# Kernel tuning notes

Measured on AMD Instinct MI355X. Metric: run time of the kernel, lower is better.

The kernel has to match this reference:

```python
import jax, jax.numpy as jnp
import numpy as np

DIM = 1024
NUM_HEADS = 16
HEAD_DIM = DIM // NUM_HEADS
ROPE_BASE = 10000.0


def _rope_cos_sin(seq_len, head_dim, dtype):
    inv_freq = 1.0 / (ROPE_BASE ** (jnp.arange(0, head_dim, 2, dtype=jnp.float32) / head_dim))
    t = jnp.arange(seq_len, dtype=jnp.float32)
    freqs = jnp.einsum('i,j->ij', t, inv_freq)          # (S, head_dim/2)
    emb = jnp.concatenate([freqs, freqs], axis=-1)       # (S, head_dim)
    return jnp.cos(emb).astype(dtype), jnp.sin(emb).astype(dtype)


def _rotate_half(x):
    x1, x2 = jnp.split(x, 2, axis=-1)
    return jnp.concatenate([-x2, x1], axis=-1)


def setup_inputs() -> dict:
    key = jax.random.key(0)
    k1, k2, k3 = jax.random.split(key, 3)
    B, S = 2, 2048
    x = jax.random.normal(k1, (B, S, DIM), dtype=jnp.float32)
    w_qkv = jax.random.normal(k2, (3 * DIM, DIM), dtype=jnp.float32) * (DIM ** -0.5)
    w_out = jax.random.normal(k3, (DIM, DIM), dtype=jnp.float32) * (DIM ** -0.5)
    return {"x": x, "w_qkv": w_qkv, "w_out": w_out}


def reference(x, w_qkv, w_out):
    B, S, _ = x.shape
    scale = HEAD_DIM ** -0.5

    qkv = jnp.einsum('bsd,ed->bse', x, w_qkv)                 # (B, S, 3*DIM)
    qkv = qkv.reshape(B, S, 3, NUM_HEADS, HEAD_DIM)
    qkv = jnp.transpose(qkv, (2, 0, 3, 1, 4))                  # (3, B, H, S, hd)
    Q, K, V = qkv[0], qkv[1], qkv[2]

    cos, sin = _rope_cos_sin(S, HEAD_DIM, x.dtype)             # (S, hd)
    Q = Q * cos + _rotate_half(Q) * sin
    K = K * cos + _rotate_half(K) * sin

    scores = jnp.einsum('bhqd,bhkd->bhqk', Q, K) * scale       # (B, H, S, S)
    causal = jnp.tril(jnp.ones((S, S), dtype=bool))
    scores = jnp.where(causal[None, None], scores, jnp.asarray(-1e9, scores.dtype))
    attn = jax.nn.softmax(scores, axis=-1)

    out = jnp.einsum('bhqk,bhkd->bhqd', attn, V)               # (B, H, S, hd)
    out = jnp.transpose(out, (0, 2, 1, 3)).reshape(B, S, DIM)
    out = jnp.einsum('bsd,ed->bse', out, w_out)
    return out
```

## Files before the change

kernel.cpp:

```cpp
#include <hip/hip_runtime.h>
#include <hip/hip_bf16.h>

#define DIM 1024
#define NHEADS 16
#define HD 64
#define BB 2
#define SS 2048
#define MTOT (BB*SS)
#define SCALE 0.125f
#define QSCALE 0.1803368801111204f

typedef __attribute__((ext_vector_type(8))) short bf16x8;
typedef __attribute__((ext_vector_type(4))) float f32x4;

__device__ __forceinline__ float bf2f(short u) {
  union { float f; unsigned int i; } v;
  v.i = ((unsigned int)(unsigned short)u) << 16;
  return v.f;
}
__device__ __forceinline__ short f2bf(float f) {
  union { float f; unsigned int i; } v; v.f = f;
  unsigned int r = v.i + 0x7fffu + ((v.i >> 16) & 1u);
  return (short)(r >> 16);
}
__device__ __forceinline__ unsigned int cvtpk_bf16(float lo, float hi) {
  unsigned int r;
  asm("v_cvt_pk_bf16_f32 %0, %1, %2" : "=v"(r) : "v"(lo), "v"(hi));
  return r;
}
__device__ __forceinline__ void async_load16(const short* g, short* l) {
  __builtin_amdgcn_global_load_lds(
      (const __attribute__((address_space(1))) unsigned int*)g,
      (__attribute__((address_space(3))) unsigned int*)l, 16, 0, 0);
}

__global__ void cvt3_kernel(const float* __restrict__ a, short* __restrict__ oa, int na,
                            const float* __restrict__ b, short* __restrict__ ob, int nb,
                            const float* __restrict__ c, short* __restrict__ oc, int nc,
                            float* __restrict__ ct, float* __restrict__ st) {
  int gid = blockIdx.x * blockDim.x + threadIdx.x;
  if (gid < SS * 32) {
    int s = gid >> 5, j = gid & 31;
    float inv = 1.0f / powf(10000.0f, (float)(2 * j) / 64.0f);
    float ang = (float)s * inv;
    ct[gid] = cosf(ang);
    st[gid] = sinf(ang);
  }
  int stride = gridDim.x * blockDim.x;
  int tot = na + nb + nc;
  for (int q = gid; q < tot; q += stride) {
    const float* src; short* dst; int off;
    if (q < na)            { src = a; dst = oa; off = q; }
    else if (q < na + nb)  { src = b; dst = ob; off = q - na; }
    else                   { src = c; dst = oc; off = q - na - nb; }
    float4 v = *(const float4*)(src + (size_t)off * 4);
    short4 o;
    o.x = f2bf(v.x); o.y = f2bf(v.y); o.z = f2bf(v.z); o.w = f2bf(v.w);
    *(short4*)(dst + (size_t)off * 4) = o;
  }
}

template<int BN, bool OUT_F32>
__global__ __launch_bounds__(256) void gemm_bt(
    const short* __restrict__ A, const short* __restrict__ B,
    void* __restrict__ C, int M, int N, int K) {
  constexpr int NFR = BN / 32;
  __shared__ __align__(16) short As[128][32];
  __shared__ __align__(16) short Bs[BN][32];
  const int nbx = N / BN;
  const int chunk = gridDim.x >> 3;
  const int wg = (blockIdx.x & 7) * chunk + (blockIdx.x >> 3);
  const int m0 = (wg / nbx) * 128, n0 = (wg % nbx) * BN;
  const int tid = threadIdx.x;
  const int lane = tid & 63;
  const int wid = tid >> 6;
  const int wm = (wid >> 1) * 64, wn = (wid & 1) * (BN / 2);
  const int row = lane & 15, kg = (lane >> 4) * 8;
  const int lrow = lane >> 2;
  const int lcol = (lane & 3) * 8;

  f32x4 acc[4][NFR];
#pragma unroll
  for (int m = 0; m < 4; m++)
#pragma unroll
    for (int n = 0; n < NFR; n++) acc[m][n] = (f32x4){0.f, 0.f, 0.f, 0.f};

  for (int kk = 0; kk < K; kk += 32) {
    __syncthreads();
#pragma unroll
    for (int i = 0; i < 2; i++) {
      int base = i * 64 + wid * 16;
      async_load16(A + (size_t)(m0 + base + lrow) * K + kk + lcol, &As[base][0]);
    }
    if constexpr (BN == 128) {
#pragma unroll
      for (int i = 0; i < 2; i++) {
        int base = i * 64 + wid * 16;
        async_load16(B + (size_t)(n0 + base + lrow) * K + kk + lcol, &Bs[base][0]);
      }
    } else {
      int base = wid * 16;
      async_load16(B + (size_t)(n0 + base + lrow) * K + kk + lcol, &Bs[base][0]);
    }
    __syncthreads();
    bf16x8 af[4], bfr[NFR];
#pragma unroll
    for (int m = 0; m < 4; m++) af[m] = *(const bf16x8*)(&As[wm + m * 16 + row][kg]);
#pragma unroll
    for (int n = 0; n < NFR; n++) bfr[n] = *(const bf16x8*)(&Bs[wn + n * 16 + row][kg]);
#pragma unroll
    for (int m = 0; m < 4; m++)
#pragma unroll
      for (int n = 0; n < NFR; n++)
        acc[m][n] = __builtin_amdgcn_mfma_f32_16x16x32_bf16(af[m], bfr[n], acc[m][n], 0, 0, 0);
  }
  const int orow = (lane >> 4) * 4, ocol = lane & 15;
#pragma unroll
  for (int m = 0; m < 4; m++)
#pragma unroll
    for (int n = 0; n < NFR; n++)
#pragma unroll
      for (int r = 0; r < 4; r++) {
        int gr = m0 + wm + m * 16 + orow + r;
        int gc = n0 + wn + n * 16 + ocol;
        if (OUT_F32) ((float*)C)[(size_t)gr * N + gc] = acc[m][n][r];
        else         ((short*)C)[(size_t)gr * N + gc] = f2bf(acc[m][n][r]);
      }
}

__global__ __launch_bounds__(256) void ropev_kernel(
    const short* __restrict__ qkv, const float* __restrict__ ct, const float* __restrict__ st,
    short* __restrict__ Q, short* __restrict__ K, short* __restrict__ Vt) {
  int bh = blockIdx.y;
  int b = bh >> 4, h = bh & 15;
  int t = threadIdx.x;
  if (blockIdx.x < SS / 64) {
    int s0 = blockIdx.x * 64;
    int rl = t >> 2;
    int d8 = (t & 3) * 8;
    int s = s0 + rl;
    size_t inbase = ((size_t)(b * SS + s)) * 3072 + h * 64 + d8;
    size_t outbase = ((size_t)bh * SS + s) * 64;
    float c[8], sn[8];
#pragma unroll
    for (int j = 0; j < 8; j++) { c[j] = ct[s * 32 + d8 + j]; sn[j] = st[s * 32 + d8 + j]; }
    {
      bf16x8 x1 = *(const bf16x8*)(qkv + inbase);
      bf16x8 x2 = *(const bf16x8*)(qkv + inbase + 32);
      bf16x8 o1, o2;
#pragma unroll
      for (int j = 0; j < 8; j++) {
        float a = bf2f(x1[j]), bb = bf2f(x2[j]);
        o1[j] = f2bf((a * c[j] - bb * sn[j]) * QSCALE);
        o2[j] = f2bf((bb * c[j] + a * sn[j]) * QSCALE);
      }
      *(bf16x8*)(Q + outbase + d8) = o1;
      *(bf16x8*)(Q + outbase + d8 + 32) = o2;
    }
    {
      bf16x8 x1 = *(const bf16x8*)(qkv + inbase + 1024);
      bf16x8 x2 = *(const bf16x8*)(qkv + inbase + 1024 + 32);
      bf16x8 o1, o2;
#pragma unroll
      for (int j = 0; j < 8; j++) {
        float a = bf2f(x1[j]), bb = bf2f(x2[j]);
        o1[j] = f2bf(a * c[j] - bb * sn[j]);
        o2[j] = f2bf(bb * c[j] + a * sn[j]);
      }
      int pc = (t & 3) ^ (s & 7);
      *(bf16x8*)(K + outbase + pc * 8) = o1;
      *(bf16x8*)(K + outbase + (pc ^ 4) * 8) = o2;
    }
  } else {
    __shared__ short ls[64][72];
    int s0 = (blockIdx.x - SS / 64) * 64;
#pragma unroll
    for (int p = 0; p < 2; p++) {
      int idx = p * 256 + t;
      int r = idx >> 3, c8 = (idx & 7) * 8;
      *(bf16x8*)(&ls[r][c8]) =
          *(const bf16x8*)(qkv + ((size_t)(b * SS + s0 + r)) * 3072 + 2048 + h * 64 + c8);
    }
    __syncthreads();
    int dl = t >> 2, sg = (t & 3) * 16;
    int c = sg >> 5, hi = (sg >> 4) & 1;
    short tmp[16];
#pragma unroll
    for (int j = 0; j < 16; j++) tmp[j] = ls[sg + j][dl];
    size_t rowbase = ((size_t)bh * 64 + dl) * SS + s0;
#pragma unroll
    for (int g = 0; g < 4; g++) {
      short4 o = { tmp[4 * g], tmp[4 * g + 1], tmp[4 * g + 2], tmp[4 * g + 3] };
      int pc = (c * 4 + g) ^ (dl & 7);
      *(short4*)(Vt + rowbase + pc * 8 + hi * 4) = o;
    }
  }
}

__global__ __launch_bounds__(256, 6) void attn_kernel(
    const short* __restrict__ Qp, const short* __restrict__ Kp, const short* __restrict__ Vt,
    short* __restrict__ O, float* __restrict__ Pf) {
  __shared__ __align__(16) short KsF[2][64 * 64];
  __shared__ __align__(16) short VsF[2][64 * 64];
  int flat = blockIdx.x;
  int wk = (flat & 7) * 128 + (flat >> 3);
  int bh = wk >> 5;
  int sub = wk & 31;
  int pr = sub >> 1, half = sub & 1;
  int b = bh >> 4, h = bh & 15;
  int tid = threadIdx.x, lane = tid & 63, w = tid >> 6;
  int row = lane & 15, grp = lane >> 4;
  const int qtH = 31 - pr;
  const int nseg = 1 + half;
  const int ck = (grp ^ (row & 7)) * 8;
  const short one_bf = (short)0x3F80;
  const bf16x8 ones = {one_bf, one_bf, one_bf, one_bf, one_bf, one_bf, one_bf, one_bf};

  const short* Kbase = Kp + (size_t)bh * SS * 64;
  const short* Vbase = Vt + (size_t)bh * 64 * SS;
  const int sr8 = lane >> 3;
  const int sc8 = (lane & 7) * 8;

  auto STAGE = [&](int bufi, int kv0) {
#pragma unroll
    for (int i = 0; i < 2; i++) {
      int rbase = i * 32 + w * 8;
      async_load16(Kbase + (size_t)(kv0 + rbase + sr8) * 64 + sc8, &KsF[bufi][rbase * 64]);
      async_load16(Vbase + (size_t)(rbase + sr8) * SS + kv0 + sc8, &VsF[bufi][rbase * 64]);
    }
  };

  const int kts0 = half ? 16 : 0;
  int cur = 0;
  STAGE(0, kts0 * 64);

#pragma unroll 1
  for (int s = 0; s < nseg; s++) {
    const int qt  = (s == 0) ? qtH : pr;
    const int kts = (s == 0) ? kts0 : 0;
    const int kte = (s == 0) ? (half ? qtH : 15) : pr;
    const bool fin = (s == 1);
    const int q0 = qt * 64;
    const int q = q0 + w * 16 + row;
    bf16x8 qf0, qf1;
    {
      size_t qb = ((size_t)bh * SS + q) * 64 + grp * 8;
      qf0 = *(const bf16x8*)(Qp + qb);
      qf1 = *(const bf16x8*)(Qp + qb + 32);
    }
    f32x4 acc[4];
    f32x4 acc2 = (f32x4){0.f, 0.f, 0.f, 0.f};
#pragma unroll
    for (int d = 0; d < 4; d++) acc[d] = (f32x4){0.f, 0.f, 0.f, 0.f};
    float m = -1e30f;

#pragma unroll 1
    for (int kt = kts; kt <= kte; kt++) {
      int kv0 = kt * 64;
      bool more = (kt < kte) || (s + 1 < nseg);
      if (more) {
        STAGE(cur ^ 1, kt < kte ? kv0 + 64 : 0);
        asm volatile("s_waitcnt vmcnt(4)" ::: "memory");
      } else {
        asm volatile("s_waitcnt vmcnt(0)" ::: "memory");
      }
      __builtin_amdgcn_sched_barrier(0);
      __builtin_amdgcn_s_barrier();
      __builtin_amdgcn_sched_barrier(0);
      const short* Kc = &KsF[cur][0];
      const short* Vc = &VsF[cur][0];

      bool last = (kt == qt);
      float sv[4][4];
      __builtin_amdgcn_s_setprio(1);
#pragma unroll
      for (int n = 0; n < 4; n++) {
        if (last && n > w) {
#pragma unroll
          for (int r = 0; r < 4; r++) sv[n][r] = -1e30f;
          continue;
        }
        f32x4 sf = (f32x4){0.f, 0.f, 0.f, 0.f};
        const short* kr_ = Kc + (n * 16 + row) * 64;
        bf16x8 kf0 = *(const bf16x8*)(kr_ + ck);
        bf16x8 kf1 = *(const bf16x8*)(kr_ + (ck ^ 32));
        sf = __builtin_amdgcn_mfma_f32_16x16x32_bf16(kf0, qf0, sf, 0, 0, 0);
        sf = __builtin_amdgcn_mfma_f32_16x16x32_bf16(kf1, qf1, sf, 0, 0, 0);
#pragma unroll
        for (int r = 0; r < 4; r++) sv[n][r] = sf[r];
      }
      __builtin_amdgcn_s_setprio(0);
      if (last) {
#pragma unroll
        for (int n = 0; n < 4; n++)
#pragma unroll
          for (int r = 0; r < 4; r++) {
            int kv = kv0 + n * 16 + grp * 4 + r;
            if (kv > q) sv[n][r] = -1e30f;
          }
      }
      float t0 = fmaxf(fmaxf(sv[0][0], sv[0][1]), sv[0][2]);
      float t1 = fmaxf(fmaxf(sv[0][3], sv[1][0]), sv[1][1]);
      float t2 = fmaxf(fmaxf(sv[1][2], sv[1][3]), sv[2][0]);
      float t3 = fmaxf(fmaxf(sv[2][1], sv[2][2]), sv[2][3]);
      float t4 = fmaxf(fmaxf(sv[3][0], sv[3][1]), sv[3][2]);
      float pmax = fmaxf(fmaxf(fmaxf(t0, t1), fmaxf(t2, t3)), fmaxf(t4, sv[3][3]));
      pmax = fmaxf(pmax, __shfl_xor(pmax, 16));
      pmax = fmaxf(pmax, __shfl_xor(pmax, 32));
      if (__any(pmax - m > 8.f)) {
        float mnew = fmaxf(m, pmax);
        float resc = __builtin_amdgcn_exp2f(m - mnew);
        m = mnew;
#pragma unroll
        for (int d = 0; d < 4; d++)
#pragma unroll
          for (int r = 0; r < 4; r++) acc[d][r] *= resc;
#pragma unroll
        for (int r = 0; r < 4; r++) acc2[r] *= resc;
      }
#pragma unroll
      for (int n = 0; n < 4; n++)
#pragma unroll
        for (int r = 0; r < 4; r++)
          sv[n][r] = __builtin_amdgcn_exp2f(sv[n][r] - m);
      __builtin_amdgcn_s_setprio(1);
#pragma unroll
      for (int c = 0; c < 2; c++) {
        union { unsigned int u[4]; bf16x8 v; } pu;
        pu.u[0] = cvtpk_bf16(sv[2 * c][0], sv[2 * c][1]);
        pu.u[1] = cvtpk_bf16(sv[2 * c][2], sv[2 * c][3]);
        pu.u[2] = cvtpk_bf16(sv[2 * c + 1][0], sv[2 * c + 1][1]);
        pu.u[3] = cvtpk_bf16(sv[2 * c + 1][2], sv[2 * c + 1][3]);
#pragma unroll
        for (int dm = 0; dm < 4; dm++) {
          const short* vr_ = Vc + (dm * 16 + row) * 64;
          bf16x8 vf = *(const bf16x8*)(vr_ + (ck ^ (c * 32)));
          acc[dm] = __builtin_amdgcn_mfma_f32_16x16x32_bf16(vf, pu.v, acc[dm], 0, 0, 0);
        }
        acc2 = __builtin_amdgcn_mfma_f32_16x16x32_bf16(ones, pu.v, acc2, 0, 0, 0);
      }
      __builtin_amdgcn_s_setprio(0);
      __builtin_amdgcn_sched_barrier(0);
      __builtin_amdgcn_s_barrier();
      __builtin_amdgcn_sched_barrier(0);
      cur ^= 1;
    }
    if (fin) {
      float linv = 1.0f / acc2[0];
      size_t ob = ((size_t)(b * SS + q)) * 1024 + h * 64 + grp * 4;
#pragma unroll
      for (int dm = 0; dm < 4; dm++) {
        union { unsigned int u[2]; short4 s4; } ou;
        ou.u[0] = cvtpk_bf16(acc[dm][0] * linv, acc[dm][1] * linv);
        ou.u[1] = cvtpk_bf16(acc[dm][2] * linv, acc[dm][3] * linv);
        *(short4*)(O + ob + dm * 16) = ou.s4;
      }
    } else {
      int slot = (bh * 16 + (qt - 16)) * 2 + half;
      float* P = Pf + (size_t)slot * 64 * 68 + (w * 16 + row) * 68;
#pragma unroll
      for (int dm = 0; dm < 4; dm++) {
        f32x4 a = acc[dm];
        *(float4*)(P + dm * 16 + grp * 4) = *(float4*)&a;
      }
      if (grp == 0) { P[64] = m; P[65] = acc2[0]; }
    }
  }
}

__global__ __launch_bounds__(64) void merge_kernel(const float* __restrict__ Pf, short* __restrict__ O) {
  int bh = blockIdx.x >> 4, ht = blockIdx.x & 15;
  int b = bh >> 4, h = bh & 15;
  int qt = ht + 16;
  int t = threadIdx.x;
  const float* p0 = Pf + ((size_t)((bh * 16 + ht) * 2)) * 64 * 68 + t * 68;
  const float* p1 = p0 + 64 * 68;
  float m0 = p0[64], l0 = p0[65], m1 = p1[64], l1 = p1[65];
  float mM = fmaxf(m0, m1);
  float e0 = __builtin_amdgcn_exp2f(m0 - mM);
  float e1 = __builtin_amdgcn_exp2f(m1 - mM);
  float linv = 1.0f / (e0 * l0 + e1 * l1);
  size_t ob = ((size_t)(b * SS + qt * 64 + t)) * 1024 + h * 64;
#pragma unroll
  for (int d8 = 0; d8 < 8; d8++) {
    float4 a0 = *(const float4*)(p0 + d8 * 8);
    float4 a1 = *(const float4*)(p1 + d8 * 8);
    float4 b0 = *(const float4*)(p0 + d8 * 8 + 4);
    float4 b1 = *(const float4*)(p1 + d8 * 8 + 4);
    union { unsigned int u[4]; short4 s4[2]; } ou;
    ou.u[0] = cvtpk_bf16((e0 * a0.x + e1 * a1.x) * linv, (e0 * a0.y + e1 * a1.y) * linv);
    ou.u[1] = cvtpk_bf16((e0 * a0.z + e1 * a1.z) * linv, (e0 * a0.w + e1 * a1.w) * linv);
    ou.u[2] = cvtpk_bf16((e0 * b0.x + e1 * b1.x) * linv, (e0 * b0.y + e1 * b1.y) * linv);
    ou.u[3] = cvtpk_bf16((e0 * b0.z + e1 * b1.z) * linv, (e0 * b0.w + e1 * b1.w) * linv);
    *(short4*)(O + ob + d8 * 8) = ou.s4[0];
    *(short4*)(O + ob + d8 * 8 + 4) = ou.s4[1];
  }
}

extern "C" void kernel_launch(void* const* d_in, const int* in_sizes, int n_in,
                              void* d_out, int out_size, void* d_ws, size_t ws_size,
                              hipStream_t stream) {
  (void)in_sizes; (void)n_in; (void)out_size; (void)ws_size;
  const float* x     = (const float*)d_in[0];
  const float* w_qkv = (const float*)d_in[1];
  const float* w_out = (const float*)d_in[2];
  float* out = (float*)d_out;

  char* ws = (char*)d_ws;
  size_t off = 0;
  auto alloc = [&](size_t bytes) -> void* {
    void* p = ws + off;
    off += (bytes + 255) & ~(size_t)255;
    return p;
  };
  short* xb    = (short*)alloc((size_t)MTOT * DIM * 2);
  short* wqkvb = (short*)alloc((size_t)3072 * 1024 * 2);
  short* woutb = (short*)alloc((size_t)1024 * 1024 * 2);
  short* qkvb  = (short*)alloc((size_t)MTOT * 3072 * 2);
  short* Qb    = (short*)alloc((size_t)32 * SS * 64 * 2);
  short* Kb    = (short*)alloc((size_t)32 * SS * 64 * 2);
  short* Vtb   = (short*)alloc((size_t)32 * 64 * SS * 2);
  float* ct    = (float*)alloc((size_t)SS * 32 * 4);
  float* st    = (float*)alloc((size_t)SS * 32 * 4);
  short* attnb = xb;
  float* Pf    = (float*)qkvb;

  cvt3_kernel<<<2048, 256, 0, stream>>>(x, xb, MTOT * DIM / 4,
                                        w_qkv, wqkvb, 3072 * 1024 / 4,
                                        w_out, woutb, 1024 * 1024 / 4, ct, st);
  gemm_bt<128, false><<<(3072 / 128) * (MTOT / 128), 256, 0, stream>>>(xb, wqkvb, qkvb, MTOT, 3072, 1024);
  ropev_kernel<<<dim3(2 * SS / 64, 32), 256, 0, stream>>>(qkvb, ct, st, Qb, Kb, Vtb);
  attn_kernel<<<1024, 256, 0, stream>>>(Qb, Kb, Vtb, attnb, Pf);
  merge_kernel<<<512, 64, 0, stream>>>(Pf, attnb);
  gemm_bt<64, true><<<(1024 / 64) * (MTOT / 128), 256, 0, stream>>>(attnb, woutb, out, MTOT, 1024, 1024);
}
```

Before: 128.1 us.

## Process two 64-row query fragments per wave to double K/V tile reuse

Each attention workgroup now handles a 128-row query tile: every wave carries two 16-row query fragments with separate softmax state. Each staged K/V tile therefore feeds twice as many MFMAs, which halves K/V loads and barriers per unit of work. The causal pairing, split-K partial layout and merge kernel are reworked for 128-row tiles, and the grid shrinks from 1024 to 512 blocks. In exchange, register pressure roughly doubles (the occupancy hint of 6 is dropped), fewer blocks cover the GPU, and some diagonal-block MFMAs are masked work.

```diff
diff --git a/kernel.cpp b/kernel.cpp
--- a/kernel.cpp
+++ b/kernel.cpp
@@ -197,20 +197,21 @@
   }
 }
 
-__global__ __launch_bounds__(256, 6) void attn_kernel(
+__global__ __launch_bounds__(256) void attn_kernel(
     const short* __restrict__ Qp, const short* __restrict__ Kp, const short* __restrict__ Vt,
     short* __restrict__ O, float* __restrict__ Pf) {
   __shared__ __align__(16) short KsF[2][64 * 64];
   __shared__ __align__(16) short VsF[2][64 * 64];
   int flat = blockIdx.x;
-  int wk = (flat & 7) * 128 + (flat >> 3);
-  int bh = wk >> 5;
-  int sub = wk & 31;
+  int wk = (flat & 7) * 64 + (flat >> 3);
+  int bh = wk >> 4;
+  int sub = wk & 15;
   int pr = sub >> 1, half = sub & 1;
   int b = bh >> 4, h = bh & 15;
   int tid = threadIdx.x, lane = tid & 63, w = tid >> 6;
   int row = lane & 15, grp = lane >> 4;
-  const int qtH = 31 - pr;
+  const int qtH = 15 - pr;
+  const int nH = 2 * qtH + 2;
   const int nseg = 1 + half;
   const int ck = (grp ^ (row & 7)) * 8;
   const short one_bf = (short)0x3F80;
@@ -230,29 +231,33 @@
     }
   };
 
-  const int kts0 = half ? 16 : 0;
   int cur = 0;
-  STAGE(0, kts0 * 64);
+  STAGE(0, (half ? 17 : 0) * 64);
 
 #pragma unroll 1
   for (int s = 0; s < nseg; s++) {
-    const int qt  = (s == 0) ? qtH : pr;
-    const int kts = (s == 0) ? kts0 : 0;
-    const int kte = (s == 0) ? (half ? qtH : 15) : pr;
+    const int qt  = s ? pr : qtH;
+    const int kts = s ? 0 : (half ? 17 : 0);
+    const int kte = s ? (2 * pr + 1) : (half ? nH - 1 : 16);
     const bool fin = (s == 1);
-    const int q0 = qt * 64;
-    const int q = q0 + w * 16 + row;
-    bf16x8 qf0, qf1;
-    {
-      size_t qb = ((size_t)bh * SS + q) * 64 + grp * 8;
-      qf0 = *(const bf16x8*)(Qp + qb);
-      qf1 = *(const bf16x8*)(Qp + qb + 32);
-    }
-    f32x4 acc[4];
-    f32x4 acc2 = (f32x4){0.f, 0.f, 0.f, 0.f};
-#pragma unroll
-    for (int d = 0; d < 4; d++) acc[d] = (f32x4){0.f, 0.f, 0.f, 0.f};
-    float m = -1e30f;
+    const int q0 = qt * 128;
+    const int qa = q0 + w * 16 + row;
+    bf16x8 qf[2][2];
+#pragma unroll
+    for (int f = 0; f < 2; f++) {
+      size_t qb_ = ((size_t)bh * SS + qa + f * 64) * 64 + grp * 8;
+      qf[f][0] = *(const bf16x8*)(Qp + qb_);
+      qf[f][1] = *(const bf16x8*)(Qp + qb_ + 32);
+    }
+    f32x4 acc[2][4];
+    f32x4 acc2[2];
+    float m[2] = {-1e30f, -1e30f};
+#pragma unroll
+    for (int f = 0; f < 2; f++) {
+      acc2[f] = (f32x4){0.f, 0.f, 0.f, 0.f};
+#pragma unroll
+      for (int d = 0; d < 4; d++) acc[f][d] = (f32x4){0.f, 0.f, 0.f, 0.f};
+    }
 
 #pragma unroll 1
     for (int kt = kts; kt <= kte; kt++) {
@@ -270,74 +275,93 @@
       const short* Kc = &KsF[cur][0];
       const short* Vc = &VsF[cur][0];
 
-      bool last = (kt == qt);
-      float sv[4][4];
+      float sv[2][4][4];
       __builtin_amdgcn_s_setprio(1);
 #pragma unroll
       for (int n = 0; n < 4; n++) {
-        if (last && n > w) {
-#pragma unroll
-          for (int r = 0; r < 4; r++) sv[n][r] = -1e30f;
-          continue;
-        }
-        f32x4 sf = (f32x4){0.f, 0.f, 0.f, 0.f};
+        int kvn = kv0 + n * 16;
         const short* kr_ = Kc + (n * 16 + row) * 64;
         bf16x8 kf0 = *(const bf16x8*)(kr_ + ck);
         bf16x8 kf1 = *(const bf16x8*)(kr_ + (ck ^ 32));
-        sf = __builtin_amdgcn_mfma_f32_16x16x32_bf16(kf0, qf0, sf, 0, 0, 0);
-        sf = __builtin_amdgcn_mfma_f32_16x16x32_bf16(kf1, qf1, sf, 0, 0, 0);
-#pragma unroll
-        for (int r = 0; r < 4; r++) sv[n][r] = sf[r];
+#pragma unroll
+        for (int f = 0; f < 2; f++) {
+          if (kvn > q0 + f * 64 + w * 16 + 15) {
+#pragma unroll
+            for (int r = 0; r < 4; r++) sv[f][n][r] = -1e30f;
+            continue;
+          }
+          f32x4 sf = (f32x4){0.f, 0.f, 0.f, 0.f};
+          sf = __builtin_amdgcn_mfma_f32_16x16x32_bf16(kf0, qf[f][0], sf, 0, 0, 0);
+          sf = __builtin_amdgcn_mfma_f32_16x16x32_bf16(kf1, qf[f][1], sf, 0, 0, 0);
+#pragma unroll
+          for (int r = 0; r < 4; r++) sv[f][n][r] = sf[r];
+        }
       }
       __builtin_amdgcn_s_setprio(0);
-      if (last) {
+#pragma unroll
+      for (int f = 0; f < 2; f++) {
+        int blo = q0 + f * 64 + w * 16;
+        int qfl = qa + f * 64;
+#pragma unroll
+        for (int n = 0; n < 4; n++) {
+          int kvn = kv0 + n * 16;
+          if (kvn <= blo + 15 && kvn + 15 > blo) {
+#pragma unroll
+            for (int r = 0; r < 4; r++) {
+              int kv = kvn + grp * 4 + r;
+              if (kv > qfl) sv[f][n][r] = -1e30f;
+            }
+          }
+        }
+      }
+#pragma unroll
+      for (int f = 0; f < 2; f++) {
+        float t0 = fmaxf(fmaxf(sv[f][0][0], sv[f][0][1]), sv[f][0][2]);
+        float t1 = fmaxf(fmaxf(sv[f][0][3], sv[f][1][0]), sv[f][1][1]);
+        float t2 = fmaxf(fmaxf(sv[f][1][2], sv[f][1][3]), sv[f][2][0]);
+        float t3 = fmaxf(fmaxf(sv[f][2][1], sv[f][2][2]), sv[f][2][3]);
+        float t4 = fmaxf(fmaxf(sv[f][3][0], sv[f][3][1]), sv[f][3][2]);
+        float pmax = fmaxf(fmaxf(fmaxf(t0, t1), fmaxf(t2, t3)), fmaxf(t4, sv[f][3][3]));
+        pmax = fmaxf(pmax, __shfl_xor(pmax, 16));
+        pmax = fmaxf(pmax, __shfl_xor(pmax, 32));
+        if (__any(pmax - m[f] > 8.f)) {
+          float mnew = fmaxf(m[f], pmax);
+          float resc = __builtin_amdgcn_exp2f(m[f] - mnew);
+          m[f] = mnew;
+#pragma unroll
+          for (int d = 0; d < 4; d++)
+#pragma unroll
+            for (int r = 0; r < 4; r++) acc[f][d][r] *= resc;
+#pragma unroll
+          for (int r = 0; r < 4; r++) acc2[f][r] *= resc;
+        }
 #pragma unroll
         for (int n = 0; n < 4; n++)
 #pragma unroll
-          for (int r = 0; r < 4; r++) {
-            int kv = kv0 + n * 16 + grp * 4 + r;
-            if (kv > q) sv[n][r] = -1e30f;
-          }
-      }
-      float t0 = fmaxf(fmaxf(sv[0][0], sv[0][1]), sv[0][2]);
-      float t1 = fmaxf(fmaxf(sv[0][3], sv[1][0]), sv[1][1]);
-      float t2 = fmaxf(fmaxf(sv[1][2], sv[1][3]), sv[2][0]);
-      float t3 = fmaxf(fmaxf(sv[2][1], sv[2][2]), sv[2][3]);
-      float t4 = fmaxf(fmaxf(sv[3][0], sv[3][1]), sv[3][2]);
-      float pmax = fmaxf(fmaxf(fmaxf(t0, t1), fmaxf(t2, t3)), fmaxf(t4, sv[3][3]));
-      pmax = fmaxf(pmax, __shfl_xor(pmax, 16));
-      pmax = fmaxf(pmax, __shfl_xor(pmax, 32));
-      if (__any(pmax - m > 8.f)) {
-        float mnew = fmaxf(m, pmax);
-        float resc = __builtin_amdgcn_exp2f(m - mnew);
-        m = mnew;
-#pragma unroll
-        for (int d = 0; d < 4; d++)
-#pragma unroll
-          for (int r = 0; r < 4; r++) acc[d][r] *= resc;
-#pragma unroll
-        for (int r = 0; r < 4; r++) acc2[r] *= resc;
-      }
-#pragma unroll
-      for (int n = 0; n < 4; n++)
-#pragma unroll
-        for (int r = 0; r < 4; r++)
-          sv[n][r] = __builtin_amdgcn_exp2f(sv[n][r] - m);
+          for (int r = 0; r < 4; r++)
+            sv[f][n][r] = __builtin_amdgcn_exp2f(sv[f][n][r] - m[f]);
+      }
       __builtin_amdgcn_s_setprio(1);
 #pragma unroll
       for (int c = 0; c < 2; c++) {
-        union { unsigned int u[4]; bf16x8 v; } pu;
-        pu.u[0] = cvtpk_bf16(sv[2 * c][0], sv[2 * c][1]);
-        pu.u[1] = cvtpk_bf16(sv[2 * c][2], sv[2 * c][3]);
-        pu.u[2] = cvtpk_bf16(sv[2 * c + 1][0], sv[2 * c + 1][1]);
-        pu.u[3] = cvtpk_bf16(sv[2 * c + 1][2], sv[2 * c + 1][3]);
+        union { unsigned int u[4]; bf16x8 v; } pu0, pu1;
+        pu0.u[0] = cvtpk_bf16(sv[0][2 * c][0], sv[0][2 * c][1]);
+        pu0.u[1] = cvtpk_bf16(sv[0][2 * c][2], sv[0][2 * c][3]);
+        pu0.u[2] = cvtpk_bf16(sv[0][2 * c + 1][0], sv[0][2 * c + 1][1]);
+        pu0.u[3] = cvtpk_bf16(sv[0][2 * c + 1][2], sv[0][2 * c + 1][3]);
+        pu1.u[0] = cvtpk_bf16(sv[1][2 * c][0], sv[1][2 * c][1]);
+        pu1.u[1] = cvtpk_bf16(sv[1][2 * c][2], sv[1][2 * c][3]);
+        pu1.u[2] = cvtpk_bf16(sv[1][2 * c + 1][0], sv[1][2 * c + 1][1]);
+        pu1.u[3] = cvtpk_bf16(sv[1][2 * c + 1][2], sv[1][2 * c + 1][3]);
 #pragma unroll
         for (int dm = 0; dm < 4; dm++) {
           const short* vr_ = Vc + (dm * 16 + row) * 64;
           bf16x8 vf = *(const bf16x8*)(vr_ + (ck ^ (c * 32)));
-          acc[dm] = __builtin_amdgcn_mfma_f32_16x16x32_bf16(vf, pu.v, acc[dm], 0, 0, 0);
-        }
-        acc2 = __builtin_amdgcn_mfma_f32_16x16x32_bf16(ones, pu.v, acc2, 0, 0, 0);
+          acc[0][dm] = __builtin_amdgcn_mfma_f32_16x16x32_bf16(vf, pu0.v, acc[0][dm], 0, 0, 0);
+          acc[1][dm] = __builtin_amdgcn_mfma_f32_16x16x32_bf16(vf, pu1.v, acc[1][dm], 0, 0, 0);
+        }
+        acc2[0] = __builtin_amdgcn_mfma_f32_16x16x32_bf16(ones, pu0.v, acc2[0], 0, 0, 0);
+        acc2[1] = __builtin_amdgcn_mfma_f32_16x16x32_bf16(ones, pu1.v, acc2[1], 0, 0, 0);
       }
       __builtin_amdgcn_s_setprio(0);
       __builtin_amdgcn_sched_barrier(0);
@@ -346,41 +370,48 @@
       cur ^= 1;
     }
     if (fin) {
-      float linv = 1.0f / acc2[0];
-      size_t ob = ((size_t)(b * SS + q)) * 1024 + h * 64 + grp * 4;
-#pragma unroll
-      for (int dm = 0; dm < 4; dm++) {
-        union { unsigned int u[2]; short4 s4; } ou;
-        ou.u[0] = cvtpk_bf16(acc[dm][0] * linv, acc[dm][1] * linv);
-        ou.u[1] = cvtpk_bf16(acc[dm][2] * linv, acc[dm][3] * linv);
-        *(short4*)(O + ob + dm * 16) = ou.s4;
+#pragma unroll
+      for (int f = 0; f < 2; f++) {
+        float linv = 1.0f / acc2[f][0];
+        size_t ob = ((size_t)(b * SS + qa + f * 64)) * 1024 + h * 64 + grp * 4;
+#pragma unroll
+        for (int dm = 0; dm < 4; dm++) {
+          union { unsigned int u[2]; short4 s4; } ou;
+          ou.u[0] = cvtpk_bf16(acc[f][dm][0] * linv, acc[f][dm][1] * linv);
+          ou.u[1] = cvtpk_bf16(acc[f][dm][2] * linv, acc[f][dm][3] * linv);
+          *(short4*)(O + ob + dm * 16) = ou.s4;
+        }
       }
     } else {
-      int slot = (bh * 16 + (qt - 16)) * 2 + half;
-      float* P = Pf + (size_t)slot * 64 * 68 + (w * 16 + row) * 68;
-#pragma unroll
-      for (int dm = 0; dm < 4; dm++) {
-        f32x4 a = acc[dm];
-        *(float4*)(P + dm * 16 + grp * 4) = *(float4*)&a;
-      }
-      if (grp == 0) { P[64] = m; P[65] = acc2[0]; }
-    }
-  }
-}
-
-__global__ __launch_bounds__(64) void merge_kernel(const float* __restrict__ Pf, short* __restrict__ O) {
-  int bh = blockIdx.x >> 4, ht = blockIdx.x & 15;
+      int slot = (bh * 8 + (qtH - 8)) * 2 + half;
+#pragma unroll
+      for (int f = 0; f < 2; f++) {
+        float* P = Pf + (size_t)slot * 128 * 68 + (f * 64 + w * 16 + row) * 68;
+#pragma unroll
+        for (int dm = 0; dm < 4; dm++) {
+          f32x4 a = acc[f][dm];
+          *(float4*)(P + dm * 16 + grp * 4) = *(float4*)&a;
+        }
+        if (grp == 0) { P[64] = m[f]; P[65] = acc2[f][0]; }
+      }
+    }
+  }
+}
+
+__global__ __launch_bounds__(128) void merge_kernel(const float* __restrict__ Pf, short* __restrict__ O) {
+  int g = blockIdx.x;
+  int bh = g >> 3, ht = g & 7;
   int b = bh >> 4, h = bh & 15;
-  int qt = ht + 16;
+  int qt = ht + 8;
   int t = threadIdx.x;
-  const float* p0 = Pf + ((size_t)((bh * 16 + ht) * 2)) * 64 * 68 + t * 68;
-  const float* p1 = p0 + 64 * 68;
+  const float* p0 = Pf + ((size_t)(g * 2)) * 128 * 68 + t * 68;
+  const float* p1 = p0 + 128 * 68;
   float m0 = p0[64], l0 = p0[65], m1 = p1[64], l1 = p1[65];
   float mM = fmaxf(m0, m1);
   float e0 = __builtin_amdgcn_exp2f(m0 - mM);
   float e1 = __builtin_amdgcn_exp2f(m1 - mM);
   float linv = 1.0f / (e0 * l0 + e1 * l1);
-  size_t ob = ((size_t)(b * SS + qt * 64 + t)) * 1024 + h * 64;
+  size_t ob = ((size_t)(b * SS + qt * 128 + t)) * 1024 + h * 64;
 #pragma unroll
   for (int d8 = 0; d8 < 8; d8++) {
     float4 a0 = *(const float4*)(p0 + d8 * 8);
@@ -430,7 +461,7 @@
                                         w_out, woutb, 1024 * 1024 / 4, ct, st);
   gemm_bt<128, false><<<(3072 / 128) * (MTOT / 128), 256, 0, stream>>>(xb, wqkvb, qkvb, MTOT, 3072, 1024);
   ropev_kernel<<<dim3(2 * SS / 64, 32), 256, 0, stream>>>(qkvb, ct, st, Qb, Kb, Vtb);
-  attn_kernel<<<1024, 256, 0, stream>>>(Qb, Kb, Vtb, attnb, Pf);
-  merge_kernel<<<512, 64, 0, stream>>>(Pf, attnb);
+  attn_kernel<<<512, 256, 0, stream>>>(Qb, Kb, Vtb, attnb, Pf);
+  merge_kernel<<<256, 128, 0, stream>>>(Pf, attnb);
   gemm_bt<64, true><<<(1024 / 64) * (MTOT / 128), 256, 0, stream>>>(attnb, woutb, out, MTOT, 1024, 1024);
 }
```

Measured after the change: 132.3 us. 1.03x slower.
